# Optimization experiments

Hardware: AMD Instinct MI355X
Metric: run time of the kernel (lower is better)

## Reference

```python
import jax, jax.numpy as jnp
import numpy as np

N, IN_DIM, EDGE_DIM = 100000, 64, 16
E = 1600000
H, C = 4, 16  # heads, out_dim per head; H*C = 64
K = 3
NEG_SLOPE = 0.2
LN_EPS = 1e-5


def setup_inputs() -> dict:
    key = jax.random.key(0)
    ks = jax.random.split(key, 16)
    s = 1.0 / np.sqrt(IN_DIM)
    se = 1.0 / np.sqrt(EDGE_DIM)
    HC = H * C
    return {
        "x": jax.random.normal(ks[0], (N, IN_DIM), jnp.float32),
        "edge_index": jax.random.randint(ks[1], (2, E), 0, N, jnp.int32),
        "edge_attr": jax.random.normal(ks[2], (E, EDGE_DIM), jnp.float32),
        "dist_to_boundary": jax.random.randint(ks[3], (N,), 0, K + 1, jnp.int32),
        # GATv2Conv params
        "W_l": jax.random.normal(ks[4], (IN_DIM, HC), jnp.float32) * s,
        "b_l": jnp.zeros((HC,), jnp.float32),
        "W_r": jax.random.normal(ks[5], (IN_DIM, HC), jnp.float32) * s,
        "b_r": jnp.zeros((HC,), jnp.float32),
        "W_e": jax.random.normal(ks[6], (EDGE_DIM, HC), jnp.float32) * se,
        "att": jax.random.normal(ks[7], (H, C), jnp.float32) * (1.0 / np.sqrt(C)),
        "bias": jnp.zeros((HC,), jnp.float32),
        # LayerNorm params
        "gamma": jnp.ones((HC,), jnp.float32),
        "beta": jnp.zeros((HC,), jnp.float32),
        # residual: in_dim == H*C -> Identity in original; identity-initialized Linear
        "W_res": jnp.eye(IN_DIM, HC, dtype=jnp.float32),
        "b_res": jnp.zeros((HC,), jnp.float32),
        "bias_per_hop": jnp.zeros((K + 1,), jnp.float32),
    }


def reference(x, edge_index, edge_attr, dist_to_boundary,
              W_l, b_l, W_r, b_r, W_e, att, bias,
              gamma, beta, W_res, b_res, bias_per_hop):
    n = x.shape[0]
    src, dst = edge_index[0], edge_index[1]

    # hop bias on edge features (module indexes edge_index[1])
    hop = jnp.clip(dist_to_boundary[dst], 0, K)
    ea = edge_attr + bias_per_hop[hop][:, None] * 0.1  # [E, edge_dim]

    # GATv2Conv (eval mode: no dropout)
    xl = (x @ W_l + b_l).reshape(n, H, C)
    xr = (x @ W_r + b_r).reshape(n, H, C)
    ee = (ea @ W_e).reshape(-1, H, C)
    m = xl[src] + xr[dst] + ee                      # [E,H,C]
    m = jnp.where(m > 0, m, NEG_SLOPE * m)          # leaky_relu
    logits = jnp.einsum('ehc,hc->eh', m, att)       # [E,H]

    # segment softmax over destination nodes
    amax = jax.ops.segment_max(logits, dst, num_segments=n)
    ex = jnp.exp(logits - amax[dst])
    den = jax.ops.segment_sum(ex, dst, num_segments=n)
    alpha = ex / (den[dst] + 1e-16)                 # [E,H]

    # weighted scatter-add of source features
    out = jax.ops.segment_sum(alpha[:, :, None] * xl[src], dst, num_segments=n)
    out = out.reshape(n, H * C) + bias

    # LayerNorm
    mu = out.mean(-1, keepdims=True)
    var = ((out - mu) ** 2).mean(-1, keepdims=True)
    out = (out - mu) / jnp.sqrt(var + LN_EPS) * gamma + beta

    # residual (Identity in original since in_dim == H*C; W_res is identity)
    return out + (x @ W_res + b_res)
```

## Files before the change

### kernel.cpp

```cpp
#include <hip/hip_runtime.h>
#include <math.h>

#define NEG_SLOPE 0.2f
#define LN_EPS 1e-5f
#define BUCKET 48

typedef __attribute__((ext_vector_type(2))) float f32x2;

template <int CTRL>
__device__ __forceinline__ float dpp_add(float x) {
    int s = __builtin_amdgcn_update_dpp(0, __float_as_int(x), CTRL, 0xF, 0xF, true);
    return x + __int_as_float(s);
}
__device__ __forceinline__ float row16_sum(float x) {
    x = dpp_add<0xB1>(x);
    x = dpp_add<0x4E>(x);
    x = dpp_add<0x124>(x);
    x = dpp_add<0x128>(x);
    return x;
}

__global__ __launch_bounds__(256) void prep(
    const float* __restrict__ x,
    const float* __restrict__ W_l, const float* __restrict__ b_l,
    const float* __restrict__ W_r, const float* __restrict__ b_r,
    const float* __restrict__ W_res, const float* __restrict__ b_res,
    const float* __restrict__ W_e,
    const int* __restrict__ dist, const float* __restrict__ bph,
    float* __restrict__ xl, float* __restrict__ xr, float* __restrict__ xres_out,
    const int* __restrict__ ei, int* __restrict__ counts, int2* __restrict__ bucket,
    int n, int E_) {
    __shared__ float sWl[4096];
    __shared__ float sWr[4096];
    __shared__ float sWs[4096];
    __shared__ float sx[256];
    for (int i = threadIdx.x; i < 4096; i += 256) {
        sWl[i] = W_l[i]; sWr[i] = W_r[i]; sWs[i] = W_res[i];
    }
    int lane = threadIdx.x & 63;
    int w = threadIdx.x >> 6;
    float bl = b_l[lane], br = b_r[lane], bs = b_res[lane];
    float wsum = 0.0f;
#pragma unroll
    for (int k = 0; k < 16; ++k) wsum += W_e[k * 64 + lane];
    __syncthreads();
    for (int base = blockIdx.x * 4; base < n; base += gridDim.x * 4) {
        __syncthreads();
        int r = base + w;
        if (r < n) sx[threadIdx.x] = x[(size_t)r * 64 + lane];
        __syncthreads();
        if (r < n) {
            float al = bl, ar = br, as_ = bs;
            const float* xv = &sx[w * 64];
#pragma unroll
            for (int k = 0; k < 64; ++k) {
                float xk = xv[k];
                al = fmaf(xk, sWl[k * 64 + lane], al);
                ar = fmaf(xk, sWr[k * 64 + lane], ar);
                as_ = fmaf(xk, sWs[k * 64 + lane], as_);
            }
            int hop = dist[r];
            hop = hop < 0 ? 0 : (hop > 3 ? 3 : hop);
            float hb = 0.1f * bph[hop];
            xl[(size_t)r * 64 + lane] = al;
            xr[(size_t)r * 64 + lane] = fmaf(hb, wsum, ar);
            xres_out[(size_t)r * 64 + lane] = as_;
        }
    }
    const int* di = ei + E_;
    for (int e = blockIdx.x * 256 + threadIdx.x; e < E_; e += gridDim.x * 256) {
        int dst = di[e];
        int src = ei[e];
        int pos = atomicAdd(&counts[dst], 1);
        pos = pos < BUCKET - 1 ? pos : BUCKET - 1;
        bucket[(size_t)dst * BUCKET + pos] = make_int2(e, src);
    }
}

#define LOAD_G(G, EA)                                                       \
    {                                                                       \
        int ec = __builtin_amdgcn_readfirstlane((EA).x);                    \
        const f32x2* p = (const f32x2*)(eattr + (size_t)ec * 16);           \
        _Pragma("unroll") for (int k = 0; k < 8; ++k) G[k] = p[k];          \
    }

#define PHASE(G, X, E, I)                                                   \
    {                                                                       \
        f32x2 mm; mm.x = X + base; mm.y = 0.0f;                             \
        _Pragma("unroll") for (int k = 0; k < 8; ++k)                       \
            mm = __builtin_elementwise_fma(G[k], w2[k], mm);                \
        float m = mm.x + mm.y;                                              \
        m = fmaxf(m, NEG_SLOPE * m);                                        \
        float l = row16_sum(m * attv);      \
        l = (I) < cnt ? l : -1e30f;                                         \
        float d = l - mref;                                                 \
        if (__any(d > 11.5f)) {                                             \
            float mnew = fmaxf(mref, l);                                    \
            float corr = exp2f(mref - mnew);                                \
            den *= corr; acc *= corr; mref = mnew; d = l - mref;            \
        }                                                                   \
        float ex = exp2f(d);                                                \
        den += ex;                                                          \
        acc = fmaf(ex, X, acc);                                             \
        X = xl[((unsigned)(E).y << 6) | lane];                              \
        LOAD_G(G, E);                                                       \
        int nx = (I) + 6; nx = nx > last ? last : nx;                       \
        E = bk[nx];                                                         \
    }

__global__ __launch_bounds__(256) void fused_gather(
    const int* __restrict__ counts, const int2* __restrict__ bucket,
    const float* __restrict__ eattr,
    const float* __restrict__ W_e, const float* __restrict__ att,
    const float* __restrict__ xl, const float* __restrict__ xr,
    const float* __restrict__ bias,
    const float* __restrict__ gamma, const float* __restrict__ beta,
    float* out, int n) {
    int lane = threadIdx.x & 63;
    float attv = att[lane] * 1.44269504f;
    float bi = bias[lane], g = gamma[lane], be = beta[lane];
    f32x2 w2[8];
#pragma unroll
    for (int k = 0; k < 8; ++k) {
        w2[k].x = W_e[(2 * k) * 64 + lane];
        w2[k].y = W_e[(2 * k + 1) * 64 + lane];
    }

    int wid = (blockIdx.x * blockDim.x + threadIdx.x) >> 6;
    int nw = (gridDim.x * blockDim.x) >> 6;
    for (int r = wid; r < n; r += nw) {
        int cnt = counts[r];
        float mref = 0.0f, den = 0.0f, acc = 0.0f;
        if (cnt > 0) {
            cnt = cnt < BUCKET ? cnt : BUCKET;
            float base = xr[((unsigned)r << 6) | lane];
            const int2* bk = bucket + (size_t)r * BUCKET;
            int last = cnt - 1;
            int i1 = 1 > last ? last : 1;
            int i2 = 2 > last ? last : 2;
            int i3 = 3 > last ? last : 3;
            int i4 = 4 > last ? last : 4;
            int i5 = 5 > last ? last : 5;
            int2 A0 = bk[0];
            int2 A1 = bk[i1];
            int2 A2 = bk[i2];
            int2 E0 = bk[i3];
            int2 E1 = bk[i4];
            int2 E2 = bk[i5];
            float X0 = xl[((unsigned)A0.y << 6) | lane];
            float X1 = xl[((unsigned)A1.y << 6) | lane];
            float X2 = xl[((unsigned)A2.y << 6) | lane];
            f32x2 G0[8], G1[8], G2[8];
            LOAD_G(G0, A0);
            LOAD_G(G1, A1);
            LOAD_G(G2, A2);
            for (int i = 0; i < cnt; i += 3) {
                PHASE(G0, X0, E0, i)
                PHASE(G1, X1, E1, i + 1)
                PHASE(G2, X2, E2, i + 2)
            }
        }
        float v = acc / (den + 1e-16f) + bi;
        float s = row16_sum(v);
        s += __shfl_xor(s, 16, 64);
        s += __shfl_xor(s, 32, 64);
        float mu = s * (1.0f / 64.0f);
        float dd = v - mu;
        float q = row16_sum(dd * dd);
        q += __shfl_xor(q, 16, 64);
        q += __shfl_xor(q, 32, 64);
        float var = q * (1.0f / 64.0f);
        float nv = dd * rsqrtf(var + LN_EPS) * g + be;
        unsigned idx = ((unsigned)r << 6) | lane;
        out[idx] = nv + out[idx];
    }
}

extern "C" void kernel_launch(void* const* d_in, const int* in_sizes, int n_in,
                              void* d_out, int out_size, void* d_ws, size_t ws_size,
                              hipStream_t stream) {
    const float* x     = (const float*)d_in[0];
    const int*   ei    = (const int*)d_in[1];
    const float* eattr = (const float*)d_in[2];
    const int*   dist  = (const int*)d_in[3];
    const float* W_l   = (const float*)d_in[4];
    const float* b_l   = (const float*)d_in[5];
    const float* W_r   = (const float*)d_in[6];
    const float* b_r   = (const float*)d_in[7];
    const float* W_e   = (const float*)d_in[8];
    const float* att   = (const float*)d_in[9];
    const float* bias  = (const float*)d_in[10];
    const float* gamma = (const float*)d_in[11];
    const float* beta  = (const float*)d_in[12];
    const float* W_res = (const float*)d_in[13];
    const float* b_res = (const float*)d_in[14];
    const float* bph   = (const float*)d_in[15];

    int n  = in_sizes[0] / 64;
    int E_ = in_sizes[1] / 2;
    float* out = (float*)d_out;

    char* ws = (char*)d_ws;
    float* xl     = (float*)ws; ws += (size_t)n * 64 * 4;
    float* xr     = (float*)ws; ws += (size_t)n * 64 * 4;
    int2*  bucket = (int2*)ws;  ws += (size_t)n * BUCKET * 8;
    int*   counts = (int*)ws;   ws += (size_t)n * 4;

    hipMemsetAsync(counts, 0, (size_t)n * 4, stream);
    prep<<<2048, 256, 0, stream>>>(x, W_l, b_l, W_r, b_r, W_res, b_res, W_e,
                                   dist, bph, xl, xr, out, ei, counts, bucket, n, E_);
    fused_gather<<<4096, 256, 0, stream>>>(counts, bucket, eattr,
                                           W_e, att, xl, xr,
                                           bias, gamma, beta, out, n);
}
```

Measured before the change: 287.0 us.

## Restructure gather prefetch to two slots with float4 edge-attribute loads

After: 438.2 us. 1.53x slower.

```diff
diff --git a/kernel.cpp b/kernel.cpp
--- a/kernel.cpp
+++ b/kernel.cpp
@@ -6,6 +6,7 @@
 #define BUCKET 48
 
 typedef __attribute__((ext_vector_type(2))) float f32x2;
+typedef __attribute__((ext_vector_type(4))) float f32x4;
 
 template <int CTRL>
 __device__ __forceinline__ float dpp_add(float x) {
@@ -77,19 +78,12 @@
     }
 }
 
-#define LOAD_G(G, EA)                                                       \
+#define PHASE(G, X, BC, BN, I)                                              \
     {                                                                       \
-        int ec = __builtin_amdgcn_readfirstlane((EA).x);                    \
-        const f32x2* p = (const f32x2*)(eattr + (size_t)ec * 16);           \
-        _Pragma("unroll") for (int k = 0; k < 8; ++k) G[k] = p[k];          \
-    }
-
-#define PHASE(G, X, E, I)                                                   \
-    {                                                                       \
-        f32x2 mm; mm.x = X + base; mm.y = 0.0f;                             \
-        _Pragma("unroll") for (int k = 0; k < 8; ++k)                       \
-            mm = __builtin_elementwise_fma(G[k], w2[k], mm);                \
-        float m = mm.x + mm.y;                                              \
+        f32x4 mm; mm.x = X + base; mm.y = 0.0f; mm.z = 0.0f; mm.w = 0.0f;   \
+        _Pragma("unroll") for (int k = 0; k < 4; ++k)                       \
+            mm = __builtin_elementwise_fma(G[k], w4[k], mm);                \
+        float m = (mm.x + mm.y) + (mm.z + mm.w);                            \
         m = fmaxf(m, NEG_SLOPE * m);                                        \
         float l = row16_sum(m * attv);      \
         l = (I) < cnt ? l : -1e30f;                                         \
@@ -102,10 +96,15 @@
         float ex = exp2f(d);                                                \
         den += ex;                                                          \
         acc = fmaf(ex, X, acc);                                             \
-        X = xl[((unsigned)(E).y << 6) | lane];                              \
-        LOAD_G(G, E);                                                       \
+        \
+        X = xl[((unsigned)(BC).y << 6) | lane];                             \
+        {                                                                   \
+            const f32x4* p = (const f32x4*)(eattr + (size_t)(BC).x * 16);   \
+            _Pragma("unroll") for (int k = 0; k < 4; ++k) G[k] = p[k];      \
+        }                                                                   \
+        BC = BN;                                                            \
         int nx = (I) + 6; nx = nx > last ? last : nx;                       \
-        E = bk[nx];                                                         \
+        BN = bk[nx];                                                        \
     }
 
 __global__ __launch_bounds__(256) void fused_gather(
@@ -119,11 +118,13 @@
     int lane = threadIdx.x & 63;
     float attv = att[lane] * 1.44269504f;
     float bi = bias[lane], g = gamma[lane], be = beta[lane];
-    f32x2 w2[8];
-#pragma unroll
-    for (int k = 0; k < 8; ++k) {
-        w2[k].x = W_e[(2 * k) * 64 + lane];
-        w2[k].y = W_e[(2 * k + 1) * 64 + lane];
+    f32x4 w4[4];
+#pragma unroll
+    for (int k = 0; k < 4; ++k) {
+        w4[k].x = W_e[(4 * k) * 64 + lane];
+        w4[k].y = W_e[(4 * k + 1) * 64 + lane];
+        w4[k].z = W_e[(4 * k + 2) * 64 + lane];
+        w4[k].w = W_e[(4 * k + 3) * 64 + lane];
     }
 
     int wid = (blockIdx.x * blockDim.x + threadIdx.x) >> 6;
@@ -136,28 +137,29 @@
             float base = xr[((unsigned)r << 6) | lane];
             const int2* bk = bucket + (size_t)r * BUCKET;
             int last = cnt - 1;
-            int i1 = 1 > last ? last : 1;
-            int i2 = 2 > last ? last : 2;
-            int i3 = 3 > last ? last : 3;
-            int i4 = 4 > last ? last : 4;
-            int i5 = 5 > last ? last : 5;
-            int2 A0 = bk[0];
-            int2 A1 = bk[i1];
-            int2 A2 = bk[i2];
-            int2 E0 = bk[i3];
-            int2 E1 = bk[i4];
-            int2 E2 = bk[i5];
-            float X0 = xl[((unsigned)A0.y << 6) | lane];
-            float X1 = xl[((unsigned)A1.y << 6) | lane];
-            float X2 = xl[((unsigned)A2.y << 6) | lane];
-            f32x2 G0[8], G1[8], G2[8];
-            LOAD_G(G0, A0);
-            LOAD_G(G1, A1);
-            LOAD_G(G2, A2);
-            for (int i = 0; i < cnt; i += 3) {
-                PHASE(G0, X0, E0, i)
-                PHASE(G1, X1, E1, i + 1)
-                PHASE(G2, X2, E2, i + 2)
+            int j1 = 1 > last ? last : 1;
+            int j2 = 2 > last ? last : 2;
+            int j3 = 3 > last ? last : 3;
+            int j4 = 4 > last ? last : 4;
+            int j5 = 5 > last ? last : 5;
+            int2 b0 = bk[0];
+            int2 b1 = bk[j1];
+            int2 Bc0 = bk[j2];
+            int2 Bc1 = bk[j3];
+            int2 Bn0 = bk[j4];
+            int2 Bn1 = bk[j5];
+            float X0 = xl[((unsigned)b0.y << 6) | lane];
+            float X1 = xl[((unsigned)b1.y << 6) | lane];
+            f32x4 G0[4], G1[4];
+            {
+                const f32x4* p0 = (const f32x4*)(eattr + (size_t)b0.x * 16);
+                const f32x4* p1 = (const f32x4*)(eattr + (size_t)b1.x * 16);
+#pragma unroll
+                for (int k = 0; k < 4; ++k) { G0[k] = p0[k]; G1[k] = p1[k]; }
+            }
+            for (int i = 0; i < cnt; i += 2) {
+                PHASE(G0, X0, Bc0, Bn0, i)
+                PHASE(G1, X1, Bc1, Bn1, i + 1)
             }
         }
         float v = acc / (den + 1e-16f) + bi;
```
